# Optimization experiments

Hardware: AMD Instinct MI355X
Metric: run time of the kernel (lower is better)

The kernel has to match this reference:

```python
import jax, jax.numpy as jnp
import numpy as np
from jax import lax

B, T, D, H, L = 512, 512, 32, 64, 2
ALPHA, BETA = 2.0 / 5.0, 4.0 / 5.0  # GRUFlowBlock contraction constants


def setup_inputs() -> dict:
    key = jax.random.key(0)
    ks = jax.random.split(key, 16)
    s = 1.0 / np.sqrt(H + 1)
    inp = {
        "x": jax.random.normal(ks[0], (B, T, D), jnp.float32),
        "t": jax.random.uniform(ks[1], (B, T, 1), jnp.float32),
        # GRU-flow layer params (spectral norm folded into weight values)
        "flow_W_hr": jax.random.normal(ks[2], (L, H, H + 1), jnp.float32) * s,
        "flow_b_hr": jax.random.normal(ks[3], (L, H), jnp.float32) * 0.01,
        "flow_W_hz": jax.random.normal(ks[4], (L, H, H + 1), jnp.float32) * s,
        "flow_b_hz": jax.random.normal(ks[5], (L, H), jnp.float32) * 0.01,
        "flow_W_hh": jax.random.normal(ks[6], (L, H, H + 1), jnp.float32) * s,
        "flow_b_hh": jax.random.normal(ks[7], (L, H), jnp.float32) * 0.01,
        # TimeTanh: tanh(w * t), per-dim scale w
        "flow_tw": jax.random.normal(ks[8], (L, H), jnp.float32),
        # nn.GRU(D, H) single layer, batch_first
        "gru_W_ih": jax.random.normal(ks[9], (3 * H, D), jnp.float32) / np.sqrt(H),
        "gru_W_hh": jax.random.normal(ks[10], (3 * H, H), jnp.float32) / np.sqrt(H),
        "gru_b_ih": jax.random.normal(ks[11], (3 * H,), jnp.float32) / np.sqrt(H),
        "gru_b_hh": jax.random.normal(ks[12], (3 * H,), jnp.float32) / np.sqrt(H),
    }
    return inp


def _flow(h, tt, flow_W_hr, flow_b_hr, flow_W_hz, flow_b_hz, flow_W_hh, flow_b_hh, flow_tw):
    # h: [B, H], tt: [B, 1]
    for l in range(L):
        inp = jnp.concatenate([h, tt], -1)  # [B, H+1]
        r = BETA * jax.nn.sigmoid(inp @ flow_W_hr[l].T + flow_b_hr[l])
        z = ALPHA * jax.nn.sigmoid(inp @ flow_W_hz[l].T + flow_b_hz[l])
        u = jnp.tanh(jnp.concatenate([r * h, tt], -1) @ flow_W_hh[l].T + flow_b_hh[l])
        h = h + jnp.tanh(flow_tw[l] * tt) * (z * (u - h))
    return h


def _gru_cell(xt, h, gru_W_ih, gru_W_hh, gru_b_ih, gru_b_hh):
    gi = xt @ gru_W_ih.T + gru_b_ih  # [B, 3H]
    gh = h @ gru_W_hh.T + gru_b_hh
    i_r, i_z, i_n = jnp.split(gi, 3, -1)
    h_r, h_z, h_n = jnp.split(gh, 3, -1)
    r = jax.nn.sigmoid(i_r + h_r)
    z = jax.nn.sigmoid(i_z + h_z)
    n = jnp.tanh(i_n + r * h_n)
    return (1.0 - z) * n + z * h


def reference(x, t, flow_W_hr, flow_b_hr, flow_W_hz, flow_b_hz, flow_W_hh, flow_b_hh,
              flow_tw, gru_W_ih, gru_W_hh, gru_b_ih, gru_b_hh):
    def step(h, xt_tt):
        xt, tt = xt_tt  # [B, D], [B, 1]
        h = _flow(h, tt, flow_W_hr, flow_b_hr, flow_W_hz, flow_b_hz,
                  flow_W_hh, flow_b_hh, flow_tw)
        h_out = h  # hiddens stores the post-flow, pre-GRU state
        h_new = _gru_cell(xt, h, gru_W_ih, gru_W_hh, gru_b_ih, gru_b_hh)
        return h_new, h_out

    h0 = jnp.zeros((x.shape[0], H), x.dtype)
    xs = (jnp.swapaxes(x, 0, 1), jnp.swapaxes(t, 0, 1))  # time-major for scan
    _, hiddens = lax.scan(step, h0, xs)  # [T, B, H]
    return jnp.swapaxes(hiddens, 0, 1)  # [B, T, H]
```

## Files before the change

kernel.cpp:

```cpp
#include <hip/hip_runtime.h>


#define NBATCH 512
#define NT     512
#define ND     32
#define NH     64
#define NL     2
#define AALPHA 0.4f
#define ABETA  0.8f

__device__ __forceinline__ float sigm(float v) {
    return __builtin_amdgcn_rcpf(1.0f + __expf(-v));
}
__device__ __forceinline__ float tanh_(float v) {
    return 1.0f - 2.0f * __builtin_amdgcn_rcpf(1.0f + __expf(2.0f * v));
}

__global__ __launch_bounds__(256, 1) void cgru_fused(
    const float* __restrict__ x, const float* __restrict__ tin,
    const float* __restrict__ Whr, const float* __restrict__ bhr,
    const float* __restrict__ Whz, const float* __restrict__ bhz,
    const float* __restrict__ Whh, const float* __restrict__ bhh,
    const float* __restrict__ tw,
    const float* __restrict__ gWih, const float* __restrict__ gWhh,
    const float* __restrict__ gbih, const float* __restrict__ gbhh,
    float* __restrict__ out)
{
    const int tid = threadIdx.x;
    const int j   = tid >> 2;
    const int q   = tid & 3;
    const int b0  = blockIdx.x * 2;

    __shared__ float hbuf[2][2][NH];
    __shared__ float rh_s[2][NH];
    __shared__ float x_s[2][ND];

    const int kh = (q & 1) * 32;
    const int xh = (q & 1) * 16;

    const float* Wrz    = (q < 2) ? Whr : Whz;
    const float* brzsrc = (q < 2) ? bhr : bhz;

    float wrz[NL][32], wu[NL][16];
    float w65rz[NL], w65u[NL], brz[NL], bu[NL], tws[NL];
#pragma unroll
    for (int l = 0; l < NL; ++l) {
        const int rowrz = (l * NH + j) * (NH + 1);
#pragma unroll
        for (int kk = 0; kk < 32; ++kk) wrz[l][kk] = Wrz[rowrz + kh + kk];
#pragma unroll
        for (int kk = 0; kk < 16; ++kk) wu[l][kk] = Whh[rowrz + q * 16 + kk];
        w65rz[l] = Wrz[rowrz + NH];
        w65u[l]  = Whh[rowrz + NH];
        brz[l]   = brzsrc[l * NH + j];
        bu[l]    = bhh[l * NH + j];
        tws[l]   = tw[l * NH + j];
    }

    const int g1row = ((q < 2) ? 0 : NH) + j;
    float g1a[16], g1b[32], g2[32];
#pragma unroll
    for (int kk = 0; kk < 16; ++kk) g1a[kk] = gWih[g1row * ND + xh + kk];
#pragma unroll
    for (int kk = 0; kk < 32; ++kk) g1b[kk] = gWhh[g1row * NH + kh + kk];
    if (q < 2) {
#pragma unroll
        for (int kk = 0; kk < 32; ++kk) g2[kk] = gWhh[(2 * NH + j) * NH + kh + kk];
    } else {
#pragma unroll
        for (int kk = 0; kk < 32; ++kk) {
            const bool use = (q == 2) ? (kk < 16) : (kk >= 16);
            g2[kk] = use ? gWih[(2 * NH + j) * ND + kk] : 0.0f;
        }
    }
    const float bg1 = gbih[g1row] + gbhh[g1row];
    const float bin = gbih[2 * NH + j];
    const float bhn = gbhh[2 * NH + j];

    if (tid < 2 * NH) (&hbuf[0][0][0])[tid] = 0.0f;
    __syncthreads();

    const float* tp0 = tin + b0 * NT;
    const float* tp1 = tin + (b0 + 1) * NT;

    for (int ts = 0; ts < NT; ++ts) {
        const int cur = ts & 1, nxt = cur ^ 1;
        const float tt0 = tp0[ts];
        const float tt1 = tp1[ts];
        float xv = 0.0f;
        if (tid < 64) xv = x[(b0 + (tid >> 5)) * (NT * ND) + ts * ND + (tid & 31)];

#pragma unroll
        for (int l = 0; l < NL; ++l) {
            float a0 = 0.0f, a1 = 0.0f;
            {
                const float* h0p = &hbuf[cur][0][kh];
                const float* h1p = &hbuf[cur][1][kh];
#pragma unroll
                for (int kk = 0; kk < 32; ++kk) {
                    a0 = fmaf(wrz[l][kk], h0p[kk], a0);
                    a1 = fmaf(wrz[l][kk], h1p[kk], a1);
                }
            }
            a0 += __shfl_xor(a0, 1);
            a1 += __shfl_xor(a1, 1);
            const float s0 = sigm(a0 + w65rz[l] * tt0 + brz[l]);
            const float s1 = sigm(a1 + w65rz[l] * tt1 + brz[l]);
            float zr0 = 0.0f, zr1 = 0.0f;
            if (q < 2) {
                if (q == 0) {
                    rh_s[0][j] = (ABETA * s0) * hbuf[cur][0][j];
                    rh_s[1][j] = (ABETA * s1) * hbuf[cur][1][j];
                }
            } else {
                zr0 = AALPHA * s0;
                zr1 = AALPHA * s1;
            }
            __syncthreads();

            float u0 = 0.0f, u1 = 0.0f;
            {
                const float* r0p = &rh_s[0][q * 16];
                const float* r1p = &rh_s[1][q * 16];
#pragma unroll
                for (int kk = 0; kk < 16; ++kk) {
                    u0 = fmaf(wu[l][kk], r0p[kk], u0);
                    u1 = fmaf(wu[l][kk], r1p[kk], u1);
                }
            }
            u0 += __shfl_xor(u0, 1); u0 += __shfl_xor(u0, 2);
            u1 += __shfl_xor(u1, 1); u1 += __shfl_xor(u1, 2);
            if (l == NL - 1 && tid < 64)
                x_s[tid >> 5][tid & 31] = xv;
            const float uu0 = tanh_(u0 + w65u[l] * tt0 + bu[l]);
            const float uu1 = tanh_(u1 + w65u[l] * tt1 + bu[l]);
            if (q >= 2) {
                const float h0 = hbuf[cur][0][j];
                const float h1 = hbuf[cur][1][j];
                const float hn0 = fmaf(tanh_(tws[l] * tt0) * zr0, uu0 - h0, h0);
                const float hn1 = fmaf(tanh_(tws[l] * tt1) * zr1, uu1 - h1, h1);
                if (q == 2) {
                    hbuf[cur][0][j] = hn0;
                    hbuf[cur][1][j] = hn1;
                    if (l == NL - 1) {
                        out[b0 * (NT * NH) + ts * NH + j]       = hn0;
                        out[(b0 + 1) * (NT * NH) + ts * NH + j] = hn1;
                    }
                }
            }
            __syncthreads();
        }

        float p0 = 0.0f, p1 = 0.0f;
        {
            const float* xp0 = &x_s[0][xh];
            const float* xp1 = &x_s[1][xh];
#pragma unroll
            for (int kk = 0; kk < 16; ++kk) {
                p0 = fmaf(g1a[kk], xp0[kk], p0);
                p1 = fmaf(g1a[kk], xp1[kk], p1);
            }
            const float* h0p = &hbuf[cur][0][kh];
            const float* h1p = &hbuf[cur][1][kh];
#pragma unroll
            for (int kk = 0; kk < 32; ++kk) {
                p0 = fmaf(g1b[kk], h0p[kk], p0);
                p1 = fmaf(g1b[kk], h1p[kk], p1);
            }
        }
        p0 += __shfl_xor(p0, 1);
        p1 += __shfl_xor(p1, 1);
        const float gate0 = sigm(p0 + bg1);
        const float gate1 = sigm(p1 + bg1);
        const float oth0 = __shfl_xor(gate0, 2);
        const float oth1 = __shfl_xor(gate1, 2);
        const float r0 = (q < 2) ? gate0 : oth0;
        const float r1 = (q < 2) ? gate1 : oth1;
        const float z0 = (q < 2) ? oth0 : gate0;
        const float z1 = (q < 2) ? oth1 : gate1;

        float d0 = 0.0f, d1 = 0.0f;
        {
            const float* s0p = (q < 2) ? &hbuf[cur][0][kh] : &x_s[0][0];
            const float* s1p = (q < 2) ? &hbuf[cur][1][kh] : &x_s[1][0];
#pragma unroll
            for (int kk = 0; kk < 32; ++kk) {
                d0 = fmaf(g2[kk], s0p[kk], d0);
                d1 = fmaf(g2[kk], s1p[kk], d1);
            }
        }
        d0 += __shfl_xor(d0, 1);
        d1 += __shfl_xor(d1, 1);
        const float e0 = __shfl_xor(d0, 2);
        const float e1 = __shfl_xor(d1, 2);
        const float hnd0 = (q < 2) ? d0 : e0;
        const float hnd1 = (q < 2) ? d1 : e1;
        const float ind0 = (q < 2) ? e0 : d0;
        const float ind1 = (q < 2) ? e1 : d1;

        const float n0 = tanh_(ind0 + bin + r0 * (hnd0 + bhn));
        const float n1 = tanh_(ind1 + bin + r1 * (hnd1 + bhn));
        const float h0 = hbuf[cur][0][j];
        const float h1 = hbuf[cur][1][j];
        const float hn0 = (1.0f - z0) * n0 + z0 * h0;
        const float hn1 = (1.0f - z1) * n1 + z1 * h1;
        if (q == 0) {
            hbuf[nxt][0][j] = hn0;
            hbuf[nxt][1][j] = hn1;
        }
        __syncthreads();
    }
}

extern "C" void kernel_launch(void* const* d_in, const int* in_sizes, int n_in,
                              void* d_out, int out_size, void* d_ws, size_t ws_size,
                              hipStream_t stream) {
    const float* x    = (const float*)d_in[0];
    const float* tin  = (const float*)d_in[1];
    const float* Whr  = (const float*)d_in[2];
    const float* bhr  = (const float*)d_in[3];
    const float* Whz  = (const float*)d_in[4];
    const float* bhz  = (const float*)d_in[5];
    const float* Whh  = (const float*)d_in[6];
    const float* bhh  = (const float*)d_in[7];
    const float* tw   = (const float*)d_in[8];
    const float* gWih = (const float*)d_in[9];
    const float* gWhh = (const float*)d_in[10];
    const float* gbih = (const float*)d_in[11];
    const float* gbhh = (const float*)d_in[12];
    float* out = (float*)d_out;

    dim3 grid(NBATCH / 2), block(256);
    hipLaunchKernelGGL(cgru_fused, grid, block, 0, stream,
                       x, tin, Whr, bhr, Whz, bhz, Whh, bhh, tw,
                       gWih, gWhh, gbih, gbhh, out);
}
```

Baseline: 1.440 ms.

## Assign one batch row per block with 8 lanes per hidden unit

The kernel now runs one batch element per block with 512 threads instead of two batch elements per 256-thread block, so 8 lanes share each hidden unit's dot products. Each lane's dot products get shorter, which shortens the serial per-timestep chain. The GRU input and hidden matvecs are merged into one 96-wide dot product over a combined h|x shared buffer. The cost is more threads doing the same work, extra shuffle reduction stages, and block-wide syncs across 512 threads.

```diff
diff --git a/kernel.cpp b/kernel.cpp
--- a/kernel.cpp
+++ b/kernel.cpp
@@ -1,13 +1,10 @@
 #include <hip/hip_runtime.h>
 
 
-#define NBATCH 512
-#define NT     512
-#define ND     32
-#define NH     64
-#define NL     2
-#define AALPHA 0.4f
-#define ABETA  0.8f
+#define NT 512
+#define ND 32
+#define NH 64
+#define NL 2
 
 __device__ __forceinline__ float sigm(float v) {
     return __builtin_amdgcn_rcpf(1.0f + __expf(-v));
@@ -16,7 +13,7 @@
     return 1.0f - 2.0f * __builtin_amdgcn_rcpf(1.0f + __expf(2.0f * v));
 }
 
-__global__ __launch_bounds__(256, 1) void cgru_fused(
+__global__ __launch_bounds__(512, 4) void cgru_fused(
     const float* __restrict__ x, const float* __restrict__ tin,
     const float* __restrict__ Whr, const float* __restrict__ bhr,
     const float* __restrict__ Whz, const float* __restrict__ bhz,
@@ -27,187 +24,136 @@
     float* __restrict__ out)
 {
     const int tid = threadIdx.x;
-    const int j   = tid >> 2;
-    const int q   = tid & 3;
-    const int b0  = blockIdx.x * 2;
+    const int j   = tid >> 3;
+    const int q   = tid & 7;
+    const int qh  = q & 3;
+    const bool isZ = q >= 4;
+    const int b   = blockIdx.x;
 
-    __shared__ float hbuf[2][2][NH];
-    __shared__ float rh_s[2][NH];
-    __shared__ float x_s[2][ND];
+    __shared__ float hS[NH];
+    __shared__ float rhS[NH];
+    __shared__ float hxS[128];
 
-    const int kh = (q & 1) * 32;
-    const int xh = (q & 1) * 16;
-
-    const float* Wrz    = (q < 2) ? Whr : Whz;
-    const float* brzsrc = (q < 2) ? bhr : bhz;
-
-    float wrz[NL][32], wu[NL][16];
+    const float* Wsrc = isZ ? Whz : Whr;
+    const float* bsrc = isZ ? bhz : bhr;
+    float wrz[NL][16], wu[NL][8];
     float w65rz[NL], w65u[NL], brz[NL], bu[NL], tws[NL];
 #pragma unroll
     for (int l = 0; l < NL; ++l) {
-        const int rowrz = (l * NH + j) * (NH + 1);
+        const int row = (l * NH + j) * (NH + 1);
 #pragma unroll
-        for (int kk = 0; kk < 32; ++kk) wrz[l][kk] = Wrz[rowrz + kh + kk];
+        for (int k = 0; k < 16; ++k) wrz[l][k] = Wsrc[row + qh * 16 + k];
 #pragma unroll
-        for (int kk = 0; kk < 16; ++kk) wu[l][kk] = Whh[rowrz + q * 16 + kk];
-        w65rz[l] = Wrz[rowrz + NH];
-        w65u[l]  = Whh[rowrz + NH];
-        brz[l]   = brzsrc[l * NH + j];
+        for (int k = 0; k < 8; ++k)  wu[l][k]  = Whh[row + q * 8 + k];
+        w65rz[l] = Wsrc[row + NH];
+        w65u[l]  = Whh[row + NH];
+        brz[l]   = bsrc[l * NH + j];
         bu[l]    = bhh[l * NH + j];
         tws[l]   = tw[l * NH + j];
     }
 
-    const int g1row = ((q < 2) ? 0 : NH) + j;
-    float g1a[16], g1b[32], g2[32];
+    const int grow = (isZ ? NH : 0) + j;
+    float g1[24];
 #pragma unroll
-    for (int kk = 0; kk < 16; ++kk) g1a[kk] = gWih[g1row * ND + xh + kk];
+    for (int k = 0; k < 24; ++k) {
+        const int m = qh * 24 + k;
+        g1[k] = (m < NH) ? gWhh[grow * NH + m] : gWih[grow * ND + (m - NH)];
+    }
+    const float bg1 = gbih[grow] + gbhh[grow];
+
+    float g2[16];
+    if (!isZ) {
 #pragma unroll
-    for (int kk = 0; kk < 32; ++kk) g1b[kk] = gWhh[g1row * NH + kh + kk];
-    if (q < 2) {
-#pragma unroll
-        for (int kk = 0; kk < 32; ++kk) g2[kk] = gWhh[(2 * NH + j) * NH + kh + kk];
+        for (int k = 0; k < 16; ++k) g2[k] = gWhh[(2 * NH + j) * NH + qh * 16 + k];
     } else {
 #pragma unroll
-        for (int kk = 0; kk < 32; ++kk) {
-            const bool use = (q == 2) ? (kk < 16) : (kk >= 16);
-            g2[kk] = use ? gWih[(2 * NH + j) * ND + kk] : 0.0f;
-        }
+        for (int k = 0; k < 8; ++k)  g2[k] = gWih[(2 * NH + j) * ND + qh * 8 + k];
+#pragma unroll
+        for (int k = 8; k < 16; ++k) g2[k] = 0.0f;
     }
-    const float bg1 = gbih[g1row] + gbhh[g1row];
     const float bin = gbih[2 * NH + j];
     const float bhn = gbhh[2 * NH + j];
 
-    if (tid < 2 * NH) (&hbuf[0][0][0])[tid] = 0.0f;
+    if (tid < NH) hS[tid] = 0.0f;
+    if (tid < 32) hxS[96 + tid] = 0.0f;
     __syncthreads();
 
-    const float* tp0 = tin + b0 * NT;
-    const float* tp1 = tin + (b0 + 1) * NT;
+    const float* xp = x + (size_t)b * NT * ND;
+    const float* tp = tin + (size_t)b * NT;
+    float* op = out + (size_t)b * NT * NH;
 
     for (int ts = 0; ts < NT; ++ts) {
-        const int cur = ts & 1, nxt = cur ^ 1;
-        const float tt0 = tp0[ts];
-        const float tt1 = tp1[ts];
+        const float tt = tp[ts];
         float xv = 0.0f;
-        if (tid < 64) xv = x[(b0 + (tid >> 5)) * (NT * ND) + ts * ND + (tid & 31)];
+        if (tid < ND) xv = xp[ts * ND + tid];
 
 #pragma unroll
         for (int l = 0; l < NL; ++l) {
-            float a0 = 0.0f, a1 = 0.0f;
+            float a = 0.0f;
             {
-                const float* h0p = &hbuf[cur][0][kh];
-                const float* h1p = &hbuf[cur][1][kh];
+                const float* hp = &hS[qh * 16];
 #pragma unroll
-                for (int kk = 0; kk < 32; ++kk) {
-                    a0 = fmaf(wrz[l][kk], h0p[kk], a0);
-                    a1 = fmaf(wrz[l][kk], h1p[kk], a1);
-                }
+                for (int k = 0; k < 16; ++k) a = fmaf(wrz[l][k], hp[k], a);
             }
-            a0 += __shfl_xor(a0, 1);
-            a1 += __shfl_xor(a1, 1);
-            const float s0 = sigm(a0 + w65rz[l] * tt0 + brz[l]);
-            const float s1 = sigm(a1 + w65rz[l] * tt1 + brz[l]);
-            float zr0 = 0.0f, zr1 = 0.0f;
-            if (q < 2) {
-                if (q == 0) {
-                    rh_s[0][j] = (ABETA * s0) * hbuf[cur][0][j];
-                    rh_s[1][j] = (ABETA * s1) * hbuf[cur][1][j];
-                }
-            } else {
-                zr0 = AALPHA * s0;
-                zr1 = AALPHA * s1;
-            }
+            a += __shfl_xor(a, 1);
+            a += __shfl_xor(a, 2);
+            const float s  = sigm(a + w65rz[l] * tt + brz[l]);
+            const float zv = 0.4f * s;
+            if (q == 0) rhS[j] = (0.8f * s) * hS[j];
             __syncthreads();
 
-            float u0 = 0.0f, u1 = 0.0f;
+            float u = 0.0f;
             {
-                const float* r0p = &rh_s[0][q * 16];
-                const float* r1p = &rh_s[1][q * 16];
+                const float* rp = &rhS[q * 8];
 #pragma unroll
-                for (int kk = 0; kk < 16; ++kk) {
-                    u0 = fmaf(wu[l][kk], r0p[kk], u0);
-                    u1 = fmaf(wu[l][kk], r1p[kk], u1);
-                }
+                for (int k = 0; k < 8; ++k) u = fmaf(wu[l][k], rp[k], u);
             }
-            u0 += __shfl_xor(u0, 1); u0 += __shfl_xor(u0, 2);
-            u1 += __shfl_xor(u1, 1); u1 += __shfl_xor(u1, 2);
-            if (l == NL - 1 && tid < 64)
-                x_s[tid >> 5][tid & 31] = xv;
-            const float uu0 = tanh_(u0 + w65u[l] * tt0 + bu[l]);
-            const float uu1 = tanh_(u1 + w65u[l] * tt1 + bu[l]);
-            if (q >= 2) {
-                const float h0 = hbuf[cur][0][j];
-                const float h1 = hbuf[cur][1][j];
-                const float hn0 = fmaf(tanh_(tws[l] * tt0) * zr0, uu0 - h0, h0);
-                const float hn1 = fmaf(tanh_(tws[l] * tt1) * zr1, uu1 - h1, h1);
-                if (q == 2) {
-                    hbuf[cur][0][j] = hn0;
-                    hbuf[cur][1][j] = hn1;
-                    if (l == NL - 1) {
-                        out[b0 * (NT * NH) + ts * NH + j]       = hn0;
-                        out[(b0 + 1) * (NT * NH) + ts * NH + j] = hn1;
-                    }
+            u += __shfl_xor(u, 1);
+            u += __shfl_xor(u, 2);
+            u += __shfl_xor(u, 4);
+            if (l == NL - 1 && tid < ND) hxS[NH + tid] = xv;
+            const float uu = tanh_(u + w65u[l] * tt + bu[l]);
+            if (q == 4) {
+                const float hj = hS[j];
+                const float hn = fmaf(tanh_(tws[l] * tt) * zv, uu - hj, hj);
+                hS[j] = hn;
+                if (l == NL - 1) {
+                    hxS[j] = hn;
+                    op[ts * NH + j] = hn;
                 }
             }
             __syncthreads();
         }
 
-        float p0 = 0.0f, p1 = 0.0f;
+        float p = 0.0f;
         {
-            const float* xp0 = &x_s[0][xh];
-            const float* xp1 = &x_s[1][xh];
+            const float* gp = &hxS[qh * 24];
 #pragma unroll
-            for (int kk = 0; kk < 16; ++kk) {
-                p0 = fmaf(g1a[kk], xp0[kk], p0);
-                p1 = fmaf(g1a[kk], xp1[kk], p1);
-            }
-            const float* h0p = &hbuf[cur][0][kh];
-            const float* h1p = &hbuf[cur][1][kh];
+            for (int k = 0; k < 24; ++k) p = fmaf(g1[k], gp[k], p);
+        }
+        p += __shfl_xor(p, 1);
+        p += __shfl_xor(p, 2);
+        const float gate = sigm(p + bg1);
+        const float oth  = __shfl_xor(gate, 4);
+        const float r = isZ ? oth : gate;
+        const float z = isZ ? gate : oth;
+
+        float d = 0.0f;
+        {
+            const float* dp = &hxS[isZ ? (NH + qh * 8) : (qh * 16)];
 #pragma unroll
-            for (int kk = 0; kk < 32; ++kk) {
-                p0 = fmaf(g1b[kk], h0p[kk], p0);
-                p1 = fmaf(g1b[kk], h1p[kk], p1);
-            }
+            for (int k = 0; k < 16; ++k) d = fmaf(g2[k], dp[k], d);
         }
-        p0 += __shfl_xor(p0, 1);
-        p1 += __shfl_xor(p1, 1);
-        const float gate0 = sigm(p0 + bg1);
-        const float gate1 = sigm(p1 + bg1);
-        const float oth0 = __shfl_xor(gate0, 2);
-        const float oth1 = __shfl_xor(gate1, 2);
-        const float r0 = (q < 2) ? gate0 : oth0;
-        const float r1 = (q < 2) ? gate1 : oth1;
-        const float z0 = (q < 2) ? oth0 : gate0;
-        const float z1 = (q < 2) ? oth1 : gate1;
+        d += __shfl_xor(d, 1);
+        d += __shfl_xor(d, 2);
+        const float e = __shfl_xor(d, 4);
+        const float hnd = isZ ? e : d;
+        const float ind = isZ ? d : e;
 
-        float d0 = 0.0f, d1 = 0.0f;
-        {
-            const float* s0p = (q < 2) ? &hbuf[cur][0][kh] : &x_s[0][0];
-            const float* s1p = (q < 2) ? &hbuf[cur][1][kh] : &x_s[1][0];
-#pragma unroll
-            for (int kk = 0; kk < 32; ++kk) {
-                d0 = fmaf(g2[kk], s0p[kk], d0);
-                d1 = fmaf(g2[kk], s1p[kk], d1);
-            }
-        }
-        d0 += __shfl_xor(d0, 1);
-        d1 += __shfl_xor(d1, 1);
-        const float e0 = __shfl_xor(d0, 2);
-        const float e1 = __shfl_xor(d1, 2);
-        const float hnd0 = (q < 2) ? d0 : e0;
-        const float hnd1 = (q < 2) ? d1 : e1;
-        const float ind0 = (q < 2) ? e0 : d0;
-        const float ind1 = (q < 2) ? e1 : d1;
-
-        const float n0 = tanh_(ind0 + bin + r0 * (hnd0 + bhn));
-        const float n1 = tanh_(ind1 + bin + r1 * (hnd1 + bhn));
-        const float h0 = hbuf[cur][0][j];
-        const float h1 = hbuf[cur][1][j];
-        const float hn0 = (1.0f - z0) * n0 + z0 * h0;
-        const float hn1 = (1.0f - z1) * n1 + z1 * h1;
-        if (q == 0) {
-            hbuf[nxt][0][j] = hn0;
-            hbuf[nxt][1][j] = hn1;
-        }
+        const float n  = tanh_(ind + bin + r * (hnd + bhn));
+        const float hj = hxS[j];
+        const float hp2 = (1.0f - z) * n + z * hj;
+        if (q == 0) hS[j] = hp2;
         __syncthreads();
     }
 }
@@ -230,7 +176,7 @@
     const float* gbhh = (const float*)d_in[12];
     float* out = (float*)d_out;
 
-    dim3 grid(NBATCH / 2), block(256);
+    dim3 grid(512), block(512);
     hipLaunchKernelGGL(cgru_fused, grid, block, 0, stream,
                        x, tin, Whr, bhr, Whz, bhz, Whh, bhh, tw,
                        gWih, gWhh, gbih, gbhh, out);
```

New measurement: 1.385 ms. 1.04x faster.
